# Kernel tuning notes

Measured on AMD Instinct MI355X. Metric: run time of the kernel, lower is better.

The kernel has to match this reference:

```python
import jax, jax.numpy as jnp
import numpy as np
import math

B, T, C, H = 2, 2048, 1024, 16
D = C // H  # head dim 64

def setup_inputs() -> dict:
    key = jax.random.key(0)
    ks = jax.random.split(key, 3)
    scale = 0.02
    return {
        "x": jax.random.normal(ks[0], (B, T, C), dtype=jnp.float32),
        "W_attn": jax.random.normal(ks[1], (C, 3 * C), dtype=jnp.float32) * scale,
        "b_attn": jnp.zeros((3 * C,), dtype=jnp.float32),
        "W_proj": jax.random.normal(ks[2], (C, C), dtype=jnp.float32) * scale,
        "b_proj": jnp.zeros((C,), dtype=jnp.float32),
    }

def reference(x, W_attn, b_attn, W_proj, b_proj):
    Bb, Tt, Cc = x.shape
    qkv = x @ W_attn + b_attn                       # [B,T,3C]
    q, k, v = jnp.split(qkv, 3, axis=-1)
    # [B,T,C] -> [B,H,T,D]
    def heads(t):
        return t.reshape(Bb, Tt, H, D).transpose(0, 2, 1, 3)
    q, k, v = heads(q), heads(k), heads(v)
    scores = jnp.einsum('bhqd,bhkd->bhqk', q, k) * (1.0 / math.sqrt(D))
    causal = jnp.tril(jnp.ones((Tt, Tt), dtype=bool))
    scores = jnp.where(causal, scores, -jnp.inf)
    attn = jax.nn.softmax(scores, axis=-1)
    out = jnp.einsum('bhqk,bhkd->bhqd', attn, v)    # [B,H,T,D]
    out = out.transpose(0, 2, 1, 3).reshape(Bb, Tt, Cc)
    return out @ W_proj + b_proj
```

## Files before the change

### kernel.cpp

```cpp
#include <hip/hip_runtime.h>

typedef unsigned short u16;
typedef unsigned int u32;
typedef float f32x4 __attribute__((ext_vector_type(4)));
typedef float f32x16 __attribute__((ext_vector_type(16)));
typedef unsigned int u32x4 __attribute__((ext_vector_type(4)));
typedef unsigned int u32x2 __attribute__((ext_vector_type(2)));
typedef unsigned short u16x8 __attribute__((ext_vector_type(8)));
typedef unsigned short u16x4 __attribute__((ext_vector_type(4)));

#define DEV static __device__ __forceinline__

constexpr int BB = 2, TT = 2048, CC = 1024, HH = 16, DD = 64;
constexpr int MDIM = BB * TT;

DEV u16 f2bf(float f) {
  unsigned int u = __builtin_bit_cast(unsigned int, f);
  u += 0x7fffu + ((u >> 16) & 1u);
  return (u16)(u >> 16);
}
DEV float bf2f(u16 h) {
  unsigned int u = ((unsigned int)h) << 16;
  return __builtin_bit_cast(float, u);
}
DEV void async16(const void* g, void* l) {
  __builtin_amdgcn_global_load_lds(
      (const __attribute__((address_space(1))) unsigned int*)g,
      (__attribute__((address_space(3))) unsigned int*)l, 16, 0, 0);
}
DEV void mfma16(f32x4& acc, u32x4 a, u32x4 b) {
  asm volatile("v_mfma_f32_16x16x32_bf16 %0, %1, %2, %0"
               : "+v"(acc)
               : "v"(a), "v"(b));
}
DEV void mfma32(f32x16& acc, u32x4 a, u32x4 b) {
  asm volatile("v_mfma_f32_32x32x16_bf16 %0, %1, %2, %0"
               : "+v"(acc)
               : "v"(a), "v"(b));
}
DEV u32 cvtpk(float lo, float hi) {
  u32 r;
  asm("v_cvt_pk_bf16_f32 %0, %1, %2" : "=v"(r) : "v"(lo), "v"(hi));
  return r;
}
DEV void pswap(u32& a, u32& b) {
#if __has_builtin(__builtin_amdgcn_permlane32_swap)
  u32x2 r = __builtin_amdgcn_permlane32_swap(a, b, false, false);
  a = r.x;
  b = r.y;
#else
  asm volatile("v_permlane32_swap_b32 %0, %1" : "+v"(a), "+v"(b));
#endif
}
DEV float exp2g(float x) {
#if __has_builtin(__builtin_amdgcn_exp2f)
  return __builtin_amdgcn_exp2f(x);
#else
  return exp2f(x);
#endif
}

__global__ void prep_all(const float* __restrict__ x,
                         const float* __restrict__ Wa, const float* __restrict__ Wp,
                         u16* __restrict__ x_bf,
                         u16* __restrict__ Wa_t, u16* __restrict__ Wp_t) {
  __shared__ float tile[32][33];
  int bx = blockIdx.x;
  const int tx = threadIdx.x, ty = threadIdx.y;
  if (bx >= 128) {
    const int cb = (bx - 128) * 32 + blockIdx.y;
    const int i = (cb * 1024 + ty * 32 + tx) * 4;
    f32x4 v = *(const f32x4*)(x + i);
    u16x4 o;
#pragma unroll
    for (int j = 0; j < 4; ++j) o[j] = f2bf(v[j]);
    *(u16x4*)(x_bf + i) = o;
    return;
  }
  const float* in;
  u16* out;
  int Cc;
  if (bx < 96) { in = Wa; out = Wa_t; Cc = 3072; }
  else { bx -= 96; in = Wp; out = Wp_t; Cc = 1024; }
  const int R = 1024;
  const int x0 = bx * 32, y0 = blockIdx.y * 32;
  tile[ty][tx] = in[(size_t)(y0 + ty) * Cc + (x0 + tx)];
  __syncthreads();
  out[(size_t)(x0 + ty) * R + (y0 + tx)] = f2bf(tile[tx][ty]);
}

__global__ __launch_bounds__(512, 2) void gemm_qkv256(
    const u16* __restrict__ A, const u16* __restrict__ Bt,
    const float* __restrict__ bias,
    u16* __restrict__ qw, u16* __restrict__ kw, u16* __restrict__ vw) {
  extern __shared__ char smem[];
  const int K = CC, NT = K / 64;
  const int tid = threadIdx.x;
  const int lane = tid & 63, w = tid >> 6;
  const int g = lane >> 4, c16 = lane & 15;
  const int wm2 = (w >> 2) * 128, wn2 = (w & 3) * 64;

  const int wgid = blockIdx.x;
  const int xcd = wgid & 7, idx = wgid >> 3;
  const int bxs = (xcd & 3) * 3 + idx % 3;
  const int bys = (xcd >> 2) * 8 + idx / 3;
  const int brow = bys * 256, bcol = bxs * 256;

  const int ssw = ((lane & 3) ^ ((lane >> 3) & 3)) << 4;
  const int rsw = (g ^ ((c16 >> 1) & 3)) << 4;

  f32x4 acc[8][4];
#pragma unroll
  for (int m = 0; m < 8; ++m)
#pragma unroll
    for (int n = 0; n < 4; ++n) acc[m][n] = f32x4{0.f, 0.f, 0.f, 0.f};

  const size_t ldb = (size_t)K * 2;
  const char* Abase = (const char*)A + (size_t)brow * ldb;
  const char* Bbase = (const char*)Bt + (size_t)bcol * ldb;

  auto STAGE = [&](int kt, int kh) {
    const int par = kt & 1;
    char* Adst = smem + (par * 2 + kh) * 16384;
    char* Bdst = smem + 65536 + (par * 2 + kh) * 16384;
    const size_t koff = (size_t)kt * 128 + kh * 64;
#pragma unroll
    for (int i = 0; i < 2; ++i) {
      const int c = w * 2 + i;
      const int row = c * 16 + (lane >> 2);
      async16(Abase + (size_t)row * ldb + koff + ssw, Adst + c * 1024);
      async16(Bbase + (size_t)row * ldb + koff + ssw, Bdst + c * 1024);
    }
  };

  STAGE(0, 0); STAGE(0, 1);
  STAGE(1, 0); STAGE(1, 1);

  for (int kt = 0; kt < NT; ++kt) {
    const int par = kt & 1;
    if (kt + 1 < NT)
      asm volatile("s_waitcnt vmcnt(8)" ::: "memory");
    else
      asm volatile("s_waitcnt vmcnt(0)" ::: "memory");
    __builtin_amdgcn_sched_barrier(0);
    __builtin_amdgcn_s_barrier();
    __builtin_amdgcn_sched_barrier(0);
#pragma unroll
    for (int kc = 0; kc < 2; ++kc) {
      const char* Ap = smem + (par * 2 + kc) * 16384;
      const char* Bp = smem + 65536 + (par * 2 + kc) * 16384;
      u32x4 af[8], bf[4];
#pragma unroll
      for (int m = 0; m < 8; ++m)
        af[m] = *(const u32x4*)(Ap + (wm2 + m * 16 + c16) * 64 + rsw);
#pragma unroll
      for (int n = 0; n < 4; ++n)
        bf[n] = *(const u32x4*)(Bp + (wn2 + n * 16 + c16) * 64 + rsw);
      asm volatile("s_waitcnt lgkmcnt(0)" ::: "memory");
      __builtin_amdgcn_sched_barrier(0);
      __builtin_amdgcn_s_setprio(1);
#pragma unroll
      for (int m = 0; m < 8; ++m)
#pragma unroll
        for (int n = 0; n < 4; ++n) mfma16(acc[m][n], af[m], bf[n]);
      __builtin_amdgcn_s_setprio(0);
      __builtin_amdgcn_s_barrier();
      if (kt + 2 < NT) STAGE(kt + 2, kc);
    }
  }

  u16* E = (u16*)smem;
  const int which = bcol >> 10;
  if (which < 2) {
#pragma unroll
    for (int n = 0; n < 4; ++n) {
      const float bv = bias[bcol + wn2 + n * 16 + c16];
#pragma unroll
      for (int m = 0; m < 8; ++m)
#pragma unroll
        for (int r = 0; r < 4; ++r)
          E[(wm2 + m * 16 + g * 4 + r) * 256 + wn2 + n * 16 + c16] =
              f2bf(acc[m][n][r] + bv);
    }
  } else {
#pragma unroll
    for (int n = 0; n < 4; ++n) {
      const float bv = bias[bcol + wn2 + n * 16 + c16];
#pragma unroll
      for (int m = 0; m < 8; ++m) {
        u16x4 t4;
#pragma unroll
        for (int r = 0; r < 4; ++r) t4[r] = f2bf(acc[m][n][r] + bv);
        *(u16x4*)&E[(wn2 + n * 16 + c16) * 256 + wm2 + m * 16 + g * 4] = t4;
      }
    }
  }
  __syncthreads();
#pragma unroll
  for (int i = 0; i < 16; ++i) {
    const int chunk = tid + i * 512;
    if (which < 2) {
      const int row = chunk >> 5;
      const int col8 = (chunk & 31) * 8;
      const int colg = bcol + col8;
      const int c = colg & 1023, h = c >> 6, d = c & 63;
      const int rowg = brow + row, b = rowg >> 11, t = rowg & (TT - 1);
      u16x8 v8 = *(const u16x8*)&E[row * 256 + col8];
      u16* dst = (which == 0 ? qw : kw) + ((size_t)(b * HH + h) * TT + t) * DD + d;
      *(u16x8*)dst = v8;
    } else {
      const int drow = chunk >> 5;
      const int t8 = (chunk & 31) * 8;
      const int colg = bcol + drow;
      const int c = colg & 1023, h = c >> 6, d = c & 63;
      const int rowg = brow + t8, b = rowg >> 11, t = rowg & (TT - 1);
      u16x8 v8 = *(const u16x8*)&E[drow * 256 + t8];
      u16* dst = vw + ((size_t)(b * HH + h) * DD + d) * TT + t;
      *(u16x8*)dst = v8;
    }
  }
}

__global__ __launch_bounds__(256) void gemm_proj(
    const u16* __restrict__ A, const u16* __restrict__ Bt,
    const float* __restrict__ bias, float* __restrict__ outF,
    int M, int N, int K) {
  __shared__ alignas(16) u16 Sh[2][128 * 64];
  u16* Asp = Sh[0];
  u16* Bsp = Sh[1];
  const int tid = threadIdx.x;
  const int lane = tid & 63, w = tid >> 6;
  const int g = lane >> 4, c16 = lane & 15;
  const int wm = (w >> 1) * 64, wn = (w & 1) * 64;

  const int wgid = blockIdx.y * gridDim.x + blockIdx.x;
  const int xcd = wgid & 7, pi = wgid >> 3;
  const int bxs = pi & 7;
  const int bys = 4 * xcd + (pi >> 3);
  const int brow = bys * 128, bcol = bxs * 128;

  const int lrow = lane >> 3;
  const int scol = ((lane & 7) ^ lrow) << 4;
  const int rswz = (c16 & 7) << 4;

  f32x4 acc[4][4];
#pragma unroll
  for (int m = 0; m < 4; ++m)
#pragma unroll
    for (int n = 0; n < 4; ++n) acc[m][n] = f32x4{0.f, 0.f, 0.f, 0.f};

  const size_t ldb = (size_t)K * 2;
  const char* Abase = (const char*)A + (size_t)brow * ldb;
  const char* Bbase = (const char*)Bt + (size_t)bcol * ldb;

  for (int kt = 0; kt < K; kt += 64) {
    __syncthreads();
#pragma unroll
    for (int i = 0; i < 4; ++i) {
      const int chunk = i * 4 + w;
      const int row = chunk * 8 + lrow;
      async16(Abase + (size_t)row * ldb + (size_t)kt * 2 + scol, (char*)Asp + chunk * 1024);
      async16(Bbase + (size_t)row * ldb + (size_t)kt * 2 + scol, (char*)Bsp + chunk * 1024);
    }
    __syncthreads();
#pragma unroll
    for (int kc = 0; kc < 2; ++kc) {
      const int cb = (kc * 64 + g * 16) ^ rswz;
      u32x4 af[4], bf8[4];
#pragma unroll
      for (int m = 0; m < 4; ++m)
        af[m] = *(const u32x4*)((const char*)Asp + (wm + m * 16 + c16) * 128 + cb);
#pragma unroll
      for (int n = 0; n < 4; ++n)
        bf8[n] = *(const u32x4*)((const char*)Bsp + (wn + n * 16 + c16) * 128 + cb);
#pragma unroll
      for (int m = 0; m < 4; ++m)
#pragma unroll
        for (int n = 0; n < 4; ++n) mfma16(acc[m][n], af[m], bf8[n]);
    }
  }

  float* Ef = (float*)&Sh[0][0];
#pragma unroll
  for (int pass = 0; pass < 2; ++pass) {
    __syncthreads();
    if ((wm >> 6) == pass) {
#pragma unroll
      for (int n = 0; n < 4; ++n) {
        const float bv = bias[bcol + wn + n * 16 + c16];
#pragma unroll
        for (int m = 0; m < 4; ++m)
#pragma unroll
          for (int r = 0; r < 4; ++r)
            Ef[(m * 16 + g * 4 + r) * 128 + wn + n * 16 + c16] = acc[m][n][r] + bv;
      }
    }
    __syncthreads();
#pragma unroll
    for (int i = 0; i < 8; ++i) {
      const int chunk = tid + i * 256;
      const int row = chunk >> 5;
      const int c4 = (chunk & 31) * 4;
      f32x4 v4 = *(const f32x4*)&Ef[row * 128 + c4];
      *(f32x4*)&outF[(size_t)(brow + pass * 64 + row) * N + bcol + c4] = v4;
    }
  }
}

__global__ __launch_bounds__(256) void attn_fwd(
    const u16* __restrict__ qw, const u16* __restrict__ kw,
    const u16* __restrict__ vw, u16* __restrict__ ao) {
  extern __shared__ u16 smem_a[];
  const int tid = threadIdx.x;
  const int lane = tid & 63, w = tid >> 6;
  const int ql = lane & 31, half = lane >> 5;
  const int bh = blockIdx.y;
  const int qb = ((bh >> 4) & 1) ? (15 - blockIdx.x) : blockIdx.x;
  const int q0w = qb * 128 + w * 32;
  const int qg = q0w + ql;
  const int lrow = lane >> 3;
  const int scol = ((lane & 7) ^ lrow) << 4;
  const int rswz = (ql & 7) << 4;

  u32x4 qf[4];
  {
    const u16* qrow = qw + ((size_t)bh * TT + qg) * DD;
    const float qs = 0.125f * 1.44269504f;
#pragma unroll
    for (int dwin = 0; dwin < 4; ++dwin) {
      u16x8 u = *(const u16x8*)(qrow + dwin * 16 + half * 8);
      u16x8 s;
#pragma unroll
      for (int j = 0; j < 8; ++j) s[j] = f2bf(bf2f(u[j]) * qs);
      qf[dwin] = __builtin_bit_cast(u32x4, s);
    }
  }

  f32x16 o0, o1;
#pragma unroll
  for (int i = 0; i < 16; ++i) { o0[i] = 0.f; o1[i] = 0.f; }
  float l_run = 0.f;

  const char* kbase = (const char*)kw + ((size_t)bh * TT) * 128;
  const char* vbase = (const char*)vw + ((size_t)bh * DD) * (TT * 2);

  const int nt = 2 * qb + 2;

  auto kptr = [&](int b) { return (char*)(smem_a + (b & 3) * 4096); };
  auto vptr = [&](int b) { return (char*)(smem_a + 16384 + (b & 3) * 4096); };

  auto STAGE = [&](int kt_) {
    if (kt_ >= nt) return;
    const int t0_ = kt_ * 64;
#pragma unroll
    for (int i_ = 0; i_ < 2; ++i_) {
      const int chunk = w * 2 + i_;
      const int row = chunk * 8 + lrow;
      async16(kbase + (size_t)(t0_ + row) * 128 + scol, kptr(kt_) + chunk * 1024);
      async16(vbase + (size_t)row * (TT * 2) + (size_t)t0_ * 2 + scol,
              vptr(kt_) + chunk * 1024);
    }
  };

  auto QK = [&](int kt_, f32x16& sa, f32x16& sb) {
    const char* Kc = kptr(kt_);
#pragma unroll
    for (int i = 0; i < 16; ++i) { sa[i] = 0.f; sb[i] = 0.f; }
    __builtin_amdgcn_s_setprio(1);
#pragma unroll
    for (int dwin = 0; dwin < 4; ++dwin) {
      const int cb = (dwin * 32 + half * 16) ^ rswz;
      u32x4 ak0 = *(const u32x4*)(Kc + (0 + ql) * 128 + cb);
      u32x4 ak1 = *(const u32x4*)(Kc + (32 + ql) * 128 + cb);
      mfma32(sa, ak0, qf[dwin]);
      mfma32(sb, ak1, qf[dwin]);
    }
    __builtin_amdgcn_s_setprio(0);
  };

  auto FINISH = [&](int kt_, f32x16& s0, f32x16& s1) {
    const int t0 = kt_ * 64;
    if (t0 >= q0w + 32) return;
    if (t0 + 63 > q0w) {
      const int kb = t0 + 4 * half - qg;
#pragma unroll
      for (int r = 0; r < 16; ++r) {
        const int ko = (r & 3) + 8 * (r >> 2);
        if (kb + ko > 0) s0[r] = -1e30f;
        if (kb + 32 + ko > 0) s1[r] = -1e30f;
      }
    }
#pragma unroll
    for (int i = 0; i < 16; ++i) {
      s0[i] = exp2g(s0[i]);
      s1[i] = exp2g(s1[i]);
    }
    float a8[8];
#pragma unroll
    for (int i = 0; i < 8; ++i)
      a8[i] = (s0[i] + s0[i + 8]) + (s1[i] + s1[i + 8]);
    float rs = ((a8[0] + a8[1]) + (a8[2] + a8[3])) + ((a8[4] + a8[5]) + (a8[6] + a8[7]));
    rs += __shfl_xor(rs, 32, 64);
    l_run += rs;

    u32x4 pf[4];
#pragma unroll
    for (int win = 0; win < 4; ++win) {
      const int b = (win & 1) * 8;
      u32 w0, w1, w2, w3;
      if (win < 2) {
        w0 = cvtpk(s0[b + 0], s0[b + 1]); w2 = cvtpk(s0[b + 4], s0[b + 5]);
        w1 = cvtpk(s0[b + 2], s0[b + 3]); w3 = cvtpk(s0[b + 6], s0[b + 7]);
      } else {
        w0 = cvtpk(s1[b + 0], s1[b + 1]); w2 = cvtpk(s1[b + 4], s1[b + 5]);
        w1 = cvtpk(s1[b + 2], s1[b + 3]); w3 = cvtpk(s1[b + 6], s1[b + 7]);
      }
      pswap(w0, w2);
      pswap(w1, w3);
      pf[win] = u32x4{w0, w1, w2, w3};
    }
    const char* Vc = vptr(kt_);
    __builtin_amdgcn_s_setprio(1);
#pragma unroll
    for (int win = 0; win < 4; ++win) {
      const int cb = (win * 32 + half * 16) ^ rswz;
      u32x4 av0 = *(const u32x4*)(Vc + (0 + ql) * 128 + cb);
      u32x4 av1 = *(const u32x4*)(Vc + (32 + ql) * 128 + cb);
      mfma32(o0, av0, pf[win]);
      mfma32(o1, av1, pf[win]);
    }
    __builtin_amdgcn_s_setprio(0);
  };

  STAGE(0);
  STAGE(1);
  STAGE(2);
  if (nt >= 3)
    asm volatile("s_waitcnt vmcnt(8)" ::: "memory");
  else
    asm volatile("s_waitcnt vmcnt(4)" ::: "memory");
  __builtin_amdgcn_sched_barrier(0);
  __builtin_amdgcn_s_barrier();
  __builtin_amdgcn_sched_barrier(0);

  f32x16 sA0, sA1, sB0, sB1;
  QK(0, sA0, sA1);

#define BODY(KT, C0, C1, N0, N1)                                          \
  {                                                                       \
    const int kt_b = (KT);                                                \
    if (kt_b + 2 < nt)                                                    \
      asm volatile("s_waitcnt vmcnt(4)" ::: "memory");                    \
    else                                                                  \
      asm volatile("s_waitcnt vmcnt(0)" ::: "memory");                    \
    __builtin_amdgcn_sched_barrier(0);                                    \
    __builtin_amdgcn_s_barrier();                                         \
    __builtin_amdgcn_sched_barrier(0);                                    \
    STAGE(kt_b + 3);                                                      \
    if (kt_b + 1 < nt && (kt_b + 1) * 64 < q0w + 32) QK(kt_b + 1, N0, N1);\
    FINISH(kt_b, C0, C1);                                                 \
  }

  for (int kt2 = 0; kt2 < nt; kt2 += 2) {
    BODY(kt2, sA0, sA1, sB0, sB1);
    BODY(kt2 + 1, sB0, sB1, sA0, sA1);
  }
#undef BODY

  const int b = bh >> 4, h = bh & 15;
  const float inv = 1.f / l_run;
  u16* aorow = ao + ((size_t)(b * TT) + qg) * CC + h * DD;
#pragma unroll
  for (int rg = 0; rg < 4; ++rg) {
    u16x4 t0v, t1v;
#pragma unroll
    for (int j = 0; j < 4; ++j) {
      t0v[j] = f2bf(o0[rg * 4 + j] * inv);
      t1v[j] = f2bf(o1[rg * 4 + j] * inv);
    }
    *(u16x4*)(aorow + 8 * rg + 4 * half) = t0v;
    *(u16x4*)(aorow + 32 + 8 * rg + 4 * half) = t1v;
  }
}

extern "C" void kernel_launch(void* const* d_in, const int* in_sizes, int n_in,
                              void* d_out, int out_size, void* d_ws, size_t ws_size,
                              hipStream_t stream) {
  const float* x  = (const float*)d_in[0];
  const float* Wa = (const float*)d_in[1];
  const float* ba = (const float*)d_in[2];
  const float* Wp = (const float*)d_in[3];
  const float* bp = (const float*)d_in[4];
  float* out = (float*)d_out;

  char* ws = (char*)d_ws;
  const size_t MB = 1ull << 20;
  u16* x_bf = (u16*)(ws);
  u16* ao   = (u16*)(ws);
  u16* Wa_t = (u16*)(ws + 8 * MB);
  u16* Wp_t = (u16*)(ws + 14 * MB);
  u16* q_ws = (u16*)(ws + 16 * MB);
  u16* k_ws = (u16*)(ws + 24 * MB);
  u16* v_ws = (u16*)(ws + 32 * MB);

  static bool attr_set = []() {
    hipFuncSetAttribute((const void*)gemm_qkv256,
                        hipFuncAttributeMaxDynamicSharedMemorySize, 131072);
    hipFuncSetAttribute((const void*)attn_fwd,
                        hipFuncAttributeMaxDynamicSharedMemorySize, 65536);
    return true;
  }();
  (void)attr_set;

  hipLaunchKernelGGL(prep_all, dim3(160, 32), dim3(32, 32), 0, stream,
                     x, Wa, Wp, x_bf, Wa_t, Wp_t);
  hipLaunchKernelGGL(gemm_qkv256, dim3(192), dim3(512), 131072, stream,
                     x_bf, Wa_t, ba, q_ws, k_ws, v_ws);
  hipLaunchKernelGGL(attn_fwd, dim3(TT / 128, BB * HH), dim3(256), 65536, stream,
                     q_ws, k_ws, v_ws, ao);
  hipLaunchKernelGGL(gemm_proj, dim3(CC / 128, MDIM / 128), dim3(256), 0, stream,
                     ao, Wp_t, bp, out, MDIM, CC, CC);
}
```

Before: 110.7 us.

## Retile QKV GEMM to 256x192 tiles filling all 256 CUs

The QKV GEMM tile changes from 256x256 to 256x192, so the grid grows from 192 to 256 workgroups and covers every CU on the 256-CU MI355X. Each pipeline stage now loads a full 128-wide K slice with a new 8-way XOR swizzle. The XCD-aware block mapping is rewritten to group 4x4 patches. The epilogue now handles tiles that straddle the Q/K/V boundary, splitting per column: q/k columns are written row-wise, and v columns are transposed with a strided gather from LDS. That gather may cause bank conflicts and adds epilogue work, and the narrower N tile lowers per-block reuse.

Measured after the change: 108.0 us. -2.4%, faster.

```diff
diff --git a/kernel.cpp b/kernel.cpp
--- a/kernel.cpp
+++ b/kernel.cpp
@@ -98,125 +98,124 @@
   const int tid = threadIdx.x;
   const int lane = tid & 63, w = tid >> 6;
   const int g = lane >> 4, c16 = lane & 15;
-  const int wm2 = (w >> 2) * 128, wn2 = (w & 3) * 64;
+  const int wm2 = (w >> 2) * 128, wn2 = (w & 3) * 48;
 
   const int wgid = blockIdx.x;
   const int xcd = wgid & 7, idx = wgid >> 3;
-  const int bxs = (xcd & 3) * 3 + idx % 3;
-  const int bys = (xcd >> 2) * 8 + idx / 3;
-  const int brow = bys * 256, bcol = bxs * 256;
-
-  const int ssw = ((lane & 3) ^ ((lane >> 3) & 3)) << 4;
-  const int rsw = (g ^ ((c16 >> 1) & 3)) << 4;
-
-  f32x4 acc[8][4];
+  const int patch = xcd * 2 + (idx >> 4);
+  const int q = idx & 15;
+  const int bys = (patch & 3) * 4 + (q & 3);
+  const int bxs = (patch >> 2) * 4 + (q >> 2);
+  const int brow = bys * 256, bcol = bxs * 192;
+
+  const int lrow = lane >> 3;
+  const int scol = ((lane & 7) ^ lrow) << 4;
+  const int rswz = (c16 & 7) << 4;
+
+  f32x4 acc[8][3];
 #pragma unroll
   for (int m = 0; m < 8; ++m)
 #pragma unroll
-    for (int n = 0; n < 4; ++n) acc[m][n] = f32x4{0.f, 0.f, 0.f, 0.f};
+    for (int n = 0; n < 3; ++n) acc[m][n] = f32x4{0.f, 0.f, 0.f, 0.f};
 
   const size_t ldb = (size_t)K * 2;
   const char* Abase = (const char*)A + (size_t)brow * ldb;
   const char* Bbase = (const char*)Bt + (size_t)bcol * ldb;
 
-  auto STAGE = [&](int kt, int kh) {
+  auto STAGE = [&](int kt) {
     const int par = kt & 1;
-    char* Adst = smem + (par * 2 + kh) * 16384;
-    char* Bdst = smem + 65536 + (par * 2 + kh) * 16384;
-    const size_t koff = (size_t)kt * 128 + kh * 64;
-#pragma unroll
-    for (int i = 0; i < 2; ++i) {
-      const int c = w * 2 + i;
-      const int row = c * 16 + (lane >> 2);
-      async16(Abase + (size_t)row * ldb + koff + ssw, Adst + c * 1024);
-      async16(Bbase + (size_t)row * ldb + koff + ssw, Bdst + c * 1024);
+    char* Adst = smem + par * 32768;
+    char* Bdst = smem + 65536 + par * 24576;
+    const size_t koff = (size_t)kt * 128;
+#pragma unroll
+    for (int i = 0; i < 4; ++i) {
+      const int c = w * 4 + i;
+      const int row = c * 8 + lrow;
+      async16(Abase + (size_t)row * ldb + koff + scol, Adst + c * 1024);
+    }
+#pragma unroll
+    for (int i = 0; i < 3; ++i) {
+      const int c = w * 3 + i;
+      const int row = c * 8 + lrow;
+      async16(Bbase + (size_t)row * ldb + koff + scol, Bdst + c * 1024);
     }
   };
 
-  STAGE(0, 0); STAGE(0, 1);
-  STAGE(1, 0); STAGE(1, 1);
+  STAGE(0);
+  STAGE(1);
 
   for (int kt = 0; kt < NT; ++kt) {
     const int par = kt & 1;
     if (kt + 1 < NT)
-      asm volatile("s_waitcnt vmcnt(8)" ::: "memory");
+      asm volatile("s_waitcnt vmcnt(7)" ::: "memory");
     else
       asm volatile("s_waitcnt vmcnt(0)" ::: "memory");
     __builtin_amdgcn_sched_barrier(0);
     __builtin_amdgcn_s_barrier();
     __builtin_amdgcn_sched_barrier(0);
+    const char* Ap = smem + par * 32768;
+    const char* Bp = smem + 65536 + par * 24576;
 #pragma unroll
     for (int kc = 0; kc < 2; ++kc) {
-      const char* Ap = smem + (par * 2 + kc) * 16384;
-      const char* Bp = smem + 65536 + (par * 2 + kc) * 16384;
-      u32x4 af[8], bf[4];
+      const int cb = (kc * 64 + g * 16) ^ rswz;
+      u32x4 af[8], bf[3];
 #pragma unroll
       for (int m = 0; m < 8; ++m)
-        af[m] = *(const u32x4*)(Ap + (wm2 + m * 16 + c16) * 64 + rsw);
-#pragma unroll
-      for (int n = 0; n < 4; ++n)
-        bf[n] = *(const u32x4*)(Bp + (wn2 + n * 16 + c16) * 64 + rsw);
+        af[m] = *(const u32x4*)(Ap + (wm2 + m * 16 + c16) * 128 + cb);
+#pragma unroll
+      for (int n = 0; n < 3; ++n)
+        bf[n] = *(const u32x4*)(Bp + (wn2 + n * 16 + c16) * 128 + cb);
       asm volatile("s_waitcnt lgkmcnt(0)" ::: "memory");
       __builtin_amdgcn_sched_barrier(0);
       __builtin_amdgcn_s_setprio(1);
 #pragma unroll
       for (int m = 0; m < 8; ++m)
 #pragma unroll
-        for (int n = 0; n < 4; ++n) mfma16(acc[m][n], af[m], bf[n]);
+        for (int n = 0; n < 3; ++n) mfma16(acc[m][n], af[m], bf[n]);
       __builtin_amdgcn_s_setprio(0);
-      __builtin_amdgcn_s_barrier();
-      if (kt + 2 < NT) STAGE(kt + 2, kc);
-    }
+    }
+    __builtin_amdgcn_s_barrier();
+    if (kt + 2 < NT) STAGE(kt + 2);
   }
 
   u16* E = (u16*)smem;
-  const int which = bcol >> 10;
-  if (which < 2) {
-#pragma unroll
-    for (int n = 0; n < 4; ++n) {
-      const float bv = bias[bcol + wn2 + n * 16 + c16];
-#pragma unroll
-      for (int m = 0; m < 8; ++m)
-#pragma unroll
-        for (int r = 0; r < 4; ++r)
-          E[(wm2 + m * 16 + g * 4 + r) * 256 + wn2 + n * 16 + c16] =
-              f2bf(acc[m][n][r] + bv);
-    }
-  } else {
-#pragma unroll
-    for (int n = 0; n < 4; ++n) {
-      const float bv = bias[bcol + wn2 + n * 16 + c16];
-#pragma unroll
-      for (int m = 0; m < 8; ++m) {
-        u16x4 t4;
-#pragma unroll
-        for (int r = 0; r < 4; ++r) t4[r] = f2bf(acc[m][n][r] + bv);
-        *(u16x4*)&E[(wn2 + n * 16 + c16) * 256 + wm2 + m * 16 + g * 4] = t4;
+#pragma unroll
+  for (int n = 0; n < 3; ++n) {
+    const float bv = bias[bcol + wn2 + n * 16 + c16];
+#pragma unroll
+    for (int m = 0; m < 8; ++m)
+#pragma unroll
+      for (int r = 0; r < 4; ++r)
+        E[(wm2 + m * 16 + g * 4 + r) * 192 + wn2 + n * 16 + c16] =
+            f2bf(acc[m][n][r] + bv);
+  }
+  __syncthreads();
+#pragma unroll
+  for (int i = 0; i < 12; ++i) {
+    const int c = tid + i * 512;
+    {
+      const int row = c / 24, col8 = (c % 24) * 8;
+      const int colg = bcol + col8;
+      if (colg < 2048) {
+        const int which = colg >> 10, cc = colg & 1023, h = cc >> 6, d = cc & 63;
+        const int rowg = brow + row, b = rowg >> 11, t = rowg & (TT - 1);
+        u16x8 v8 = *(const u16x8*)&E[row * 192 + col8];
+        u16* dst = (which == 0 ? qw : kw) + ((size_t)(b * HH + h) * TT + t) * DD + d;
+        *(u16x8*)dst = v8;
       }
     }
-  }
-  __syncthreads();
-#pragma unroll
-  for (int i = 0; i < 16; ++i) {
-    const int chunk = tid + i * 512;
-    if (which < 2) {
-      const int row = chunk >> 5;
-      const int col8 = (chunk & 31) * 8;
-      const int colg = bcol + col8;
-      const int c = colg & 1023, h = c >> 6, d = c & 63;
-      const int rowg = brow + row, b = rowg >> 11, t = rowg & (TT - 1);
-      u16x8 v8 = *(const u16x8*)&E[row * 256 + col8];
-      u16* dst = (which == 0 ? qw : kw) + ((size_t)(b * HH + h) * TT + t) * DD + d;
-      *(u16x8*)dst = v8;
-    } else {
-      const int drow = chunk >> 5;
-      const int t8 = (chunk & 31) * 8;
-      const int colg = bcol + drow;
-      const int c = colg & 1023, h = c >> 6, d = c & 63;
-      const int rowg = brow + t8, b = rowg >> 11, t = rowg & (TT - 1);
-      u16x8 v8 = *(const u16x8*)&E[drow * 256 + t8];
-      u16* dst = vw + ((size_t)(b * HH + h) * DD + d) * TT + t;
-      *(u16x8*)dst = v8;
+    {
+      const int col = c % 192, row8 = (c / 192) * 8;
+      const int colg = bcol + col;
+      if (colg >= 2048) {
+        const int cc = colg & 1023, h = cc >> 6, d = cc & 63;
+        const int rowg = brow + row8, b = rowg >> 11, t = rowg & (TT - 1);
+        u16x8 v8;
+#pragma unroll
+        for (int j = 0; j < 8; ++j) v8[j] = E[(row8 + j) * 192 + col];
+        u16* dst = vw + ((size_t)(b * HH + h) * DD + d) * TT + t;
+        *(u16x8*)dst = v8;
+      }
     }
   }
 }
@@ -505,7 +504,7 @@
 
   static bool attr_set = []() {
     hipFuncSetAttribute((const void*)gemm_qkv256,
-                        hipFuncAttributeMaxDynamicSharedMemorySize, 131072);
+                        hipFuncAttributeMaxDynamicSharedMemorySize, 114688);
     hipFuncSetAttribute((const void*)attn_fwd,
                         hipFuncAttributeMaxDynamicSharedMemorySize, 65536);
     return true;
@@ -514,7 +513,7 @@
 
   hipLaunchKernelGGL(prep_all, dim3(160, 32), dim3(32, 32), 0, stream,
                      x, Wa, Wp, x_bf, Wa_t, Wp_t);
-  hipLaunchKernelGGL(gemm_qkv256, dim3(192), dim3(512), 131072, stream,
+  hipLaunchKernelGGL(gemm_qkv256, dim3(256), dim3(512), 114688, stream,
                      x_bf, Wa_t, ba, q_ws, k_ws, v_ws);
   hipLaunchKernelGGL(attn_fwd, dim3(TT / 128, BB * HH), dim3(256), 65536, stream,
                      q_ws, k_ws, v_ws, ao);
```
